# Kernel tuning notes

Measured on AMD Instinct MI355X. Metric: run time of the kernel, lower is better.

The kernel has to match this reference:

```python
import jax, jax.numpy as jnp
import numpy as np

# MX microscaling spec: block_size=32 shared power-of-2 scale, int8 elements (MXINT8),
# vector (SIMD) ops rounded to bfloat16 as in microxcaling's simd_* / vec_* ops.
BLOCK = 32
BITS = 8  # int8 element format: grid step 2^(shared_exp - (BITS-2)), range [-2^(BITS-1), 2^(BITS-1)-1]


def bf16_round(x):
    # bfloat=16 rounding used by simd_split / simd_add / vec ops
    return x.astype(jnp.bfloat16).astype(jnp.float32)


def mx_quant(x):
    """MXINT8 fake-quant along last (contraction) axis with block-shared exponent.
    Straight-through estimator for gradients."""
    s = x.shape
    xb = x.reshape(s[:-1] + (s[-1] // BLOCK, BLOCK))
    amax = jnp.max(jnp.abs(xb), axis=-1, keepdims=True)
    shared_exp = jnp.floor(jnp.log2(jnp.where(amax > 0, amax, 1.0)))
    scale = jnp.exp2(shared_exp - (BITS - 2))
    q = jnp.clip(jnp.round(xb / scale), -(2.0 ** (BITS - 1)), 2.0 ** (BITS - 1) - 1) * scale
    q = jnp.where(amax > 0, q, 0.0).reshape(s)
    return x + jax.lax.stop_gradient(q - x)


def mx_linear(x, W, b):
    # quantize activations and weights to MX blocks along K, fp32 accumulate, bf16 bias-add
    y = jnp.einsum('btk,ok->bto', mx_quant(x), mx_quant(W))
    return bf16_round(y + b)


def mx_layernorm(x, w, b, eps=1e-5):
    mu = jnp.mean(x, axis=-1, keepdims=True)
    var = jnp.mean(jnp.square(x - mu), axis=-1, keepdims=True)
    return bf16_round((x - mu) * jax.lax.rsqrt(var + eps) * w + b)


def mx_gelu(x):
    # tanh-approx gelu as in microxcaling, bf16-rounded output
    c = jnp.float32(0.7978845608028654)  # sqrt(2/pi)
    return bf16_round(0.5 * x * (1.0 + jnp.tanh(c * (x + 0.044715 * x * x * x))))


def setup_inputs() -> dict:
    key = jax.random.key(0)
    ks = jax.random.split(key, 5)
    B, S, H = 2, 2048, 2048
    inputs = jax.random.normal(ks[0], (B, S, H), dtype=jnp.float32)
    ln_w = jnp.ones((H,), dtype=jnp.float32)
    ln_b = jnp.zeros((H,), dtype=jnp.float32)
    W1 = jax.random.normal(ks[1], (4 * H, H), dtype=jnp.float32) * (1.0 / np.sqrt(H))
    b1 = jnp.zeros((4 * H,), dtype=jnp.float32)
    W2 = jax.random.normal(ks[2], (H, 4 * H), dtype=jnp.float32) * (1.0 / np.sqrt(4 * H))
    b2 = jnp.zeros((H,), dtype=jnp.float32)
    return {"inputs": inputs, "ln_w": ln_w, "ln_b": ln_b, "W1": W1, "b1": b1, "W2": W2, "b2": b2}


def reference(inputs, ln_w, ln_b, W1, b1, W2, b2):
    # simd_split: bf16-rounded copies for MLP branch and residual branch
    x = bf16_round(inputs)
    residual = bf16_round(inputs)
    h = mx_layernorm(x, ln_w, ln_b)
    h = mx_linear(h, W1, b1)          # [B,S,4H]
    h = mx_gelu(h)
    h = mx_linear(h, W2, b2)          # [B,S,H]
    return bf16_round(residual + h)    # simd_add
```

## Files before the change

kernel.cpp:

```cpp
#include <hip/hip_runtime.h>

#define DEVI __device__ __forceinline__

typedef __bf16 bf16x8 __attribute__((ext_vector_type(8)));
typedef float f32x4 __attribute__((ext_vector_type(4)));

DEVI unsigned short f2bf(float f) {
  unsigned u = __float_as_uint(f);
  u = (u + 0x7FFFu + ((u >> 16) & 1u)) >> 16;
  return (unsigned short)u;
}
DEVI float bf2f(unsigned short h) { return __uint_as_float(((unsigned)h) << 16); }
DEVI float bf16r(float f) { return bf2f(f2bf(f)); }

DEVI void mx_scales(float amax, float& scale, float& inv) {
  unsigned eb = __float_as_uint(amax) & 0x7f800000u;
  scale = __uint_as_float(eb - (6u << 23));
  inv   = __uint_as_float((260u << 23) - eb);
}

DEVI unsigned short quantv(float v, float scale, float inv) {
  float qv = rintf(v * inv);
  qv = fminf(fmaxf(qv, -128.f), 127.f);
  return f2bf(qv * scale);
}

DEVI void quant8(const float* h, float amax, unsigned short* q) {
  if (amax > 0.f) {
    float scale, inv;
    mx_scales(amax, scale, inv);
#pragma unroll
    for (int k = 0; k < 8; ++k) q[k] = quantv(h[k], scale, inv);
  } else {
#pragma unroll
    for (int k = 0; k < 8; ++k) q[k] = 0;
  }
}

DEVI void gl2lds16(const void* g, void* l) {
  __builtin_amdgcn_global_load_lds(
      (__attribute__((address_space(1))) void*)const_cast<void*>(g),
      (__attribute__((address_space(3))) void*)l, 16, 0, 0);
}

DEVI uint4 pack8(const unsigned short* q) {
  uint4 o;
  o.x = (unsigned)q[0] | ((unsigned)q[1] << 16);
  o.y = (unsigned)q[2] | ((unsigned)q[3] << 16);
  o.z = (unsigned)q[4] | ((unsigned)q[5] << 16);
  o.w = (unsigned)q[6] | ((unsigned)q[7] << 16);
  return o;
}

__global__ __launch_bounds__(256) void prep_k(const float* __restrict__ W1,
                                              const float* __restrict__ W2,
                                              const float* __restrict__ X,
                                              const float* __restrict__ lw,
                                              const float* __restrict__ lb,
                                              unsigned short* __restrict__ qW1,
                                              unsigned short* __restrict__ qW2,
                                              unsigned short* __restrict__ a1) {
  __shared__ float red[4];
  const int bid = blockIdx.x;
  const int t = threadIdx.x;
  if (bid < 16384) {
    const float* src = (bid < 8192) ? W1 : W2;
    unsigned short* dst = (bid < 8192) ? qW1 : qW2;
    size_t idx = (size_t)(bid & 8191) * 256 + t;
    float4 v0 = ((const float4*)src)[idx * 2];
    float4 v1 = ((const float4*)src)[idx * 2 + 1];
    float h[8] = {v0.x, v0.y, v0.z, v0.w, v1.x, v1.y, v1.z, v1.w};
    float amax = 0.f;
#pragma unroll
    for (int k = 0; k < 8; ++k) amax = fmaxf(amax, fabsf(h[k]));
    amax = fmaxf(amax, __shfl_xor(amax, 1));
    amax = fmaxf(amax, __shfl_xor(amax, 2));
    unsigned short q[8];
    quant8(h, amax, q);
    ((uint4*)dst)[idx] = pack8(q);
  } else {
    const int H = 2048;
    const int row = bid - 16384;
    const int lane = t & 63, wave = t >> 6;
    const float* xr = X + (size_t)row * H;
    float4 v0 = ((const float4*)xr)[2 * t];
    float4 v1 = ((const float4*)xr)[2 * t + 1];
    float x[8] = {bf16r(v0.x), bf16r(v0.y), bf16r(v0.z), bf16r(v0.w),
                  bf16r(v1.x), bf16r(v1.y), bf16r(v1.z), bf16r(v1.w)};
    float s = 0.f;
#pragma unroll
    for (int k = 0; k < 8; ++k) s += x[k];
#pragma unroll
    for (int o = 32; o; o >>= 1) s += __shfl_xor(s, o);
    if (lane == 0) red[wave] = s;
    __syncthreads();
    float mu = (red[0] + red[1] + red[2] + red[3]) * (1.0f / H);
    __syncthreads();
    float v = 0.f;
#pragma unroll
    for (int k = 0; k < 8; ++k) { float d = x[k] - mu; v += d * d; }
#pragma unroll
    for (int o = 32; o; o >>= 1) v += __shfl_xor(v, o);
    if (lane == 0) red[wave] = v;
    __syncthreads();
    float var = (red[0] + red[1] + red[2] + red[3]) * (1.0f / H);
    float rstd = 1.0f / sqrtf(var + 1e-5f);
    float h[8];
    float amax = 0.f;
#pragma unroll
    for (int k = 0; k < 8; ++k) {
      int col = t * 8 + k;
      h[k] = bf16r((x[k] - mu) * rstd * lw[col] + lb[col]);
      amax = fmaxf(amax, fabsf(h[k]));
    }
    amax = fmaxf(amax, __shfl_xor(amax, 1));
    amax = fmaxf(amax, __shfl_xor(amax, 2));
    unsigned short q[8];
    quant8(h, amax, q);
    ((uint4*)(a1 + (size_t)row * H))[t] = pack8(q);
  }
}

__global__ __launch_bounds__(256) void quant_bf16_ip(unsigned short* __restrict__ X) {
  size_t idx = (size_t)blockIdx.x * 256 + threadIdx.x;
  uint4 v = ((const uint4*)X)[idx];
  unsigned short u[8] = {(unsigned short)(v.x & 0xffff), (unsigned short)(v.x >> 16),
                         (unsigned short)(v.y & 0xffff), (unsigned short)(v.y >> 16),
                         (unsigned short)(v.z & 0xffff), (unsigned short)(v.z >> 16),
                         (unsigned short)(v.w & 0xffff), (unsigned short)(v.w >> 16)};
  float h[8];
#pragma unroll
  for (int k = 0; k < 8; ++k) h[k] = bf2f(u[k]);
  float amax = 0.f;
#pragma unroll
  for (int k = 0; k < 8; ++k) amax = fmaxf(amax, fabsf(h[k]));
  amax = fmaxf(amax, __shfl_xor(amax, 1));
  amax = fmaxf(amax, __shfl_xor(amax, 2));
  unsigned short q[8];
  quant8(h, amax, q);
  ((uint4*)X)[idx] = pack8(q);
}

template <int MODE>
__global__ __launch_bounds__(256) void gemm_mx(const unsigned short* __restrict__ A,
                                               const unsigned short* __restrict__ B,
                                               int M, int N, int K,
                                               const float* __restrict__ bias,
                                               const float* __restrict__ resid,
                                               void* __restrict__ outp) {
  __shared__ unsigned short As[128 * 64];
  __shared__ unsigned short Bs[128 * 64];

  const int tid = threadIdx.x;
  const int lane = tid & 63;
  const int wave = tid >> 6;
  const int wr = (wave >> 1) * 64;
  const int wc = (wave & 1) * 64;
  const int lr = lane & 15;
  const int quad = lane >> 4;

  const int m0 = blockIdx.y * 128;
  const int n0 = blockIdx.x * 128;

  size_t aoff[4], boff[4];
  int lbase[4];
#pragma unroll
  for (int j = 0; j < 4; ++j) {
    int n = j * 256 + tid;
    int r = n >> 3, c = (n & 7) ^ (r & 7);
    aoff[j] = (size_t)(m0 + r) * K + (size_t)c * 8;
    boff[j] = (size_t)(n0 + r) * K + (size_t)c * 8;
    lbase[j] = (j * 256 + (tid & ~63)) * 8;
  }

  f32x4 acc[4][4];
#pragma unroll
  for (int i = 0; i < 4; ++i)
#pragma unroll
    for (int j = 0; j < 4; ++j) acc[i][j] = (f32x4){0.f, 0.f, 0.f, 0.f};

  for (int k0 = 0; k0 < K; k0 += 64) {
#pragma unroll
    for (int j = 0; j < 4; ++j) gl2lds16(A + aoff[j] + k0, As + lbase[j]);
#pragma unroll
    for (int j = 0; j < 4; ++j) gl2lds16(B + boff[j] + k0, Bs + lbase[j]);
    __syncthreads();
#pragma unroll
    for (int s = 0; s < 2; ++s) {
      bf16x8 af[4], bfr[4];
#pragma unroll
      for (int i = 0; i < 4; ++i) {
        int row = wr + i * 16 + lr;
        int ch = (s * 4 + quad) ^ (row & 7);
        af[i] = *(const bf16x8*)(As + row * 64 + ch * 8);
      }
#pragma unroll
      for (int j = 0; j < 4; ++j) {
        int row = wc + j * 16 + lr;
        int ch = (s * 4 + quad) ^ (row & 7);
        bfr[j] = *(const bf16x8*)(Bs + row * 64 + ch * 8);
      }
#pragma unroll
      for (int i = 0; i < 4; ++i)
#pragma unroll
        for (int j = 0; j < 4; ++j)
          acc[i][j] = __builtin_amdgcn_mfma_f32_16x16x32_bf16(af[i], bfr[j], acc[i][j], 0, 0, 0);
    }
    __syncthreads();
  }

#pragma unroll
  for (int i = 0; i < 4; ++i) {
#pragma unroll
    for (int j = 0; j < 4; ++j) {
#pragma unroll
      for (int r = 0; r < 4; ++r) {
        int gm = m0 + wr + i * 16 + quad * 4 + r;
        int gn = n0 + wc + j * 16 + lr;
        float y = acc[i][j][r];
        if (MODE == 1) {
          float t = bf16r(y + bias[gn]);
          float u2 = 1.5957691216057308f * (t + 0.044715f * t * t * t);
          float E = __expf(u2);
          float th = 1.0f - 2.0f / (E + 1.0f);
          float g = 0.5f * t * (1.0f + th);
          ((unsigned short*)outp)[(size_t)gm * N + gn] = f2bf(g);
        } else {
          float h = bf16r(y + bias[gn]);
          float rr = bf16r(resid[(size_t)gm * N + gn]);
          ((float*)outp)[(size_t)gm * N + gn] = bf16r(rr + h);
        }
      }
    }
  }
  (void)M;
}

extern "C" void kernel_launch(void* const* d_in, const int* in_sizes, int n_in,
                              void* d_out, int out_size, void* d_ws, size_t ws_size,
                              hipStream_t stream) {
  const float* inputs = (const float*)d_in[0];
  const float* ln_w   = (const float*)d_in[1];
  const float* ln_b   = (const float*)d_in[2];
  const float* W1     = (const float*)d_in[3];
  const float* b1     = (const float*)d_in[4];
  const float* W2     = (const float*)d_in[5];
  const float* b2     = (const float*)d_in[6];
  float* out = (float*)d_out;
  char* ws = (char*)d_ws;
  (void)in_sizes; (void)n_in; (void)out_size; (void)ws_size;

  unsigned short* qW1  = (unsigned short*)(ws);
  unsigned short* qW2  = (unsigned short*)(ws + (size_t)33554432);
  unsigned short* a1   = (unsigned short*)(ws + (size_t)67108864);
  unsigned short* act2 = (unsigned short*)(ws + (size_t)83886080);

  const int M = 4096;

  prep_k<<<20480, 256, 0, stream>>>(W1, W2, inputs, ln_w, ln_b, qW1, qW2, a1);

  gemm_mx<1><<<dim3(8192 / 128, M / 128), 256, 0, stream>>>(
      a1, qW1, M, 8192, 2048, b1, nullptr, (void*)act2);

  quant_bf16_ip<<<16384, 256, 0, stream>>>(act2);

  gemm_mx<2><<<dim3(2048 / 128, M / 128), 256, 0, stream>>>(
      act2, qW2, M, 2048, 8192, b2, inputs, (void*)out);
}
```

Before: 523.7 us.

## Fuse MX quantization of GELU output into first GEMM epilogue

Removes the separate in-place quantization kernel for the intermediate activation and instead computes the 32-element block amax in the GEMM1 epilogue. It uses DPP row reductions across the 16 lanes of a row, pairing two 16-column fragments per block. This saves a full read and write pass over the 4096x8192 bf16 intermediate plus one kernel launch. In exchange the epilogue gets more work: the cross-lane reductions and a switch from the __expf-based tanh to tanhf.

```diff
diff --git a/kernel.cpp b/kernel.cpp
--- a/kernel.cpp
+++ b/kernel.cpp
@@ -35,6 +35,19 @@
 #pragma unroll
     for (int k = 0; k < 8; ++k) q[k] = 0;
   }
+}
+
+template <int N>
+DEVI float qmax_step(float x) {
+  int y = __builtin_amdgcn_update_dpp(0, __float_as_int(x), 0x120 | N, 0xF, 0xF, true);
+  return fmaxf(x, __int_as_float(y));
+}
+DEVI float quad_row_max(float x) {
+  x = qmax_step<1>(x);
+  x = qmax_step<2>(x);
+  x = qmax_step<4>(x);
+  x = qmax_step<8>(x);
+  return x;
 }
 
 DEVI void gl2lds16(const void* g, void* l) {
@@ -121,26 +134,6 @@
   }
 }
 
-__global__ __launch_bounds__(256) void quant_bf16_ip(unsigned short* __restrict__ X) {
-  size_t idx = (size_t)blockIdx.x * 256 + threadIdx.x;
-  uint4 v = ((const uint4*)X)[idx];
-  unsigned short u[8] = {(unsigned short)(v.x & 0xffff), (unsigned short)(v.x >> 16),
-                         (unsigned short)(v.y & 0xffff), (unsigned short)(v.y >> 16),
-                         (unsigned short)(v.z & 0xffff), (unsigned short)(v.z >> 16),
-                         (unsigned short)(v.w & 0xffff), (unsigned short)(v.w >> 16)};
-  float h[8];
-#pragma unroll
-  for (int k = 0; k < 8; ++k) h[k] = bf2f(u[k]);
-  float amax = 0.f;
-#pragma unroll
-  for (int k = 0; k < 8; ++k) amax = fmaxf(amax, fabsf(h[k]));
-  amax = fmaxf(amax, __shfl_xor(amax, 1));
-  amax = fmaxf(amax, __shfl_xor(amax, 2));
-  unsigned short q[8];
-  quant8(h, amax, q);
-  ((uint4*)X)[idx] = pack8(q);
-}
-
 template <int MODE>
 __global__ __launch_bounds__(256) void gemm_mx(const unsigned short* __restrict__ A,
                                                const unsigned short* __restrict__ B,
@@ -209,24 +202,45 @@
     __syncthreads();
   }
 
-#pragma unroll
-  for (int i = 0; i < 4; ++i) {
-#pragma unroll
-    for (int j = 0; j < 4; ++j) {
+  if (MODE == 1) {
+#pragma unroll
+    for (int i = 0; i < 4; ++i) {
 #pragma unroll
       for (int r = 0; r < 4; ++r) {
-        int gm = m0 + wr + i * 16 + quad * 4 + r;
-        int gn = n0 + wc + j * 16 + lr;
-        float y = acc[i][j][r];
-        if (MODE == 1) {
-          float t = bf16r(y + bias[gn]);
-          float u2 = 1.5957691216057308f * (t + 0.044715f * t * t * t);
-          float E = __expf(u2);
-          float th = 1.0f - 2.0f / (E + 1.0f);
-          float g = 0.5f * t * (1.0f + th);
-          ((unsigned short*)outp)[(size_t)gm * N + gn] = f2bf(g);
-        } else {
-          float h = bf16r(y + bias[gn]);
+        const int gm = m0 + wr + i * 16 + quad * 4 + r;
+        float g[4];
+#pragma unroll
+        for (int j = 0; j < 4; ++j) {
+          float t = bf16r(acc[i][j][r] + bias[n0 + wc + j * 16 + lr]);
+          float u = 0.7978845608028654f * (t + 0.044715f * t * t * t);
+          g[j] = bf16r(0.5f * t * (1.0f + tanhf(u)));
+        }
+        float a = quad_row_max(fmaxf(fabsf(g[0]), fabsf(g[1])));
+        float b = quad_row_max(fmaxf(fabsf(g[2]), fabsf(g[3])));
+        unsigned short q[4];
+        if (a > 0.f) {
+          float sc, iv; mx_scales(a, sc, iv);
+          q[0] = quantv(g[0], sc, iv); q[1] = quantv(g[1], sc, iv);
+        } else { q[0] = q[1] = 0; }
+        if (b > 0.f) {
+          float sc, iv; mx_scales(b, sc, iv);
+          q[2] = quantv(g[2], sc, iv); q[3] = quantv(g[3], sc, iv);
+        } else { q[2] = q[3] = 0; }
+        unsigned short* orow = (unsigned short*)outp + (size_t)gm * N + n0 + wc + lr;
+#pragma unroll
+        for (int j = 0; j < 4; ++j) orow[j * 16] = q[j];
+      }
+    }
+  } else {
+#pragma unroll
+    for (int i = 0; i < 4; ++i) {
+#pragma unroll
+      for (int j = 0; j < 4; ++j) {
+#pragma unroll
+        for (int r = 0; r < 4; ++r) {
+          int gm = m0 + wr + i * 16 + quad * 4 + r;
+          int gn = n0 + wc + j * 16 + lr;
+          float h = bf16r(acc[i][j][r] + bias[gn]);
           float rr = bf16r(resid[(size_t)gm * N + gn]);
           ((float*)outp)[(size_t)gm * N + gn] = bf16r(rr + h);
         }
@@ -262,8 +276,6 @@
   gemm_mx<1><<<dim3(8192 / 128, M / 128), 256, 0, stream>>>(
       a1, qW1, M, 8192, 2048, b1, nullptr, (void*)act2);
 
-  quant_bf16_ip<<<16384, 256, 0, stream>>>(act2);
-
   gemm_mx<2><<<dim3(2048 / 128, M / 128), 256, 0, stream>>>(
       act2, qW2, M, 2048, 8192, b2, inputs, (void*)out);
 }
```

Result: faster. 503.6 us (-3.8%).
